# Kernel tuning notes

Hardware: AMD Instinct MI355X
Metric: run time of the kernel (lower is better)

The kernel has to match this reference:

```python
import jax, jax.numpy as jnp
import numpy as np

B, T, DIM, HEADS, DH = 4, 2048, 1024, 16, 64  # dh = dim // heads


def setup_inputs() -> dict:
    key = jax.random.key(0)
    k1, k2, k3 = jax.random.split(key, 3)
    x = jax.random.normal(k1, (B, T, DIM), dtype=jnp.float32)
    # nn.Linear weights, stored as [in, out] for x @ W convention
    W_qkv = jax.random.normal(k2, (DIM, 3 * HEADS * DH), dtype=jnp.float32) * (DIM ** -0.5)
    W_o = jax.random.normal(k3, (HEADS * DH, DIM), dtype=jnp.float32) * ((HEADS * DH) ** -0.5)
    return {"x": x, "W_qkv": W_qkv, "W_o": W_o}


def reference(x, W_qkv, W_o):
    b, t, _ = x.shape
    qkv = x @ W_qkv  # [b, t, 3*h*dh]
    # einops 'b t (d k h) -> k b h t d' with k=3, h=HEADS: fused axis splits as (dh, 3, h)
    qkv = qkv.reshape(b, t, DH, 3, HEADS)
    qkv = jnp.transpose(qkv, (3, 0, 4, 1, 2))  # [3, b, h, t, dh]
    q, k, v = qkv[0], qkv[1], qkv[2]
    scale = DH ** -0.5
    scores = jnp.einsum('bhid,bhjd->bhij', q, k) * scale  # [b, h, t, t]
    attn = jax.nn.softmax(scores, axis=-1)
    out = jnp.einsum('bhij,bhjd->bhid', attn, v)  # [b, h, t, dh]
    out = jnp.transpose(out, (0, 2, 1, 3)).reshape(b, t, HEADS * DH)  # 'b h t d -> b t (h d)'
    return out @ W_o
```

## Files before the change

### kernel.cpp

```cpp
#include <hip/hip_runtime.h>

typedef __bf16 bf16;
typedef __bf16 bf16x4 __attribute__((ext_vector_type(4)));
typedef __bf16 bf16x8 __attribute__((ext_vector_type(8)));
typedef float  f32x4  __attribute__((ext_vector_type(4)));
typedef unsigned int u32;
typedef unsigned int u32x2 __attribute__((ext_vector_type(2)));
typedef unsigned int u32x4 __attribute__((ext_vector_type(4)));

#define LOG2E 1.44269504088896340736f
#define EXP_SC (0.125f * LOG2E)

#if __has_builtin(__builtin_amdgcn_exp2f)
#define EXP2F(x) __builtin_amdgcn_exp2f(x)
#else
#define EXP2F(x) __builtin_exp2f(x)
#endif

__device__ __forceinline__ u32 pk_bf16(float lo, float hi) {
  u32 a = __float_as_uint(lo) + 0x8000u;
  u32 b = __float_as_uint(hi) + 0x8000u;
  return __builtin_amdgcn_perm(b, a, 0x07060302);
}
__device__ __forceinline__ unsigned short bf16r(float x) {
  return (unsigned short)((__float_as_uint(x) + 0x8000u) >> 16);
}

__device__ __forceinline__ void async_ld16(void* lds, const void* g) {
  __builtin_amdgcn_global_load_lds(
      (const __attribute__((address_space(1))) void*)(g),
      (__attribute__((address_space(3))) void*)(lds),
      16, 0, 0);
}

__global__ void convert_x(const float* __restrict__ x, bf16* __restrict__ xb) {
  int i = blockIdx.x * 256 + threadIdx.x;
  float4 v = ((const float4*)x)[i];
  u32x2 o = { pk_bf16(v.x, v.y), pk_bf16(v.z, v.w) };
  *(u32x2*)(xb + (size_t)i * 4) = o;
}

__global__ void prep_wqkv(const float* __restrict__ W, bf16* __restrict__ WT) {
  __shared__ float s[4 * 3072];
  const int k0 = blockIdx.x * 4;
  for (int i = threadIdx.x; i < 3072; i += 256) {
    int r = i / 768, c = (i - r * 768) * 4;
    *(float4*)(s + r * 3072 + c) = *(const float4*)(W + (size_t)(k0 + r) * 3072 + c);
  }
  __syncthreads();
  for (int n = threadIdx.x; n < 3072; n += 256) {
    int d = n & 63, h = (n >> 6) & 15, wch = n >> 10;
    int on = d * 48 + wch * 16 + h;
    u32x2 v = { pk_bf16(s[0 * 3072 + on], s[1 * 3072 + on]),
                pk_bf16(s[2 * 3072 + on], s[3 * 3072 + on]) };
    *(u32x2*)(WT + (size_t)n * 1024 + k0) = v;
  }
}

__global__ void prep_wo(const float* __restrict__ W, bf16* __restrict__ WT) {
  __shared__ float s[8 * 1024];
  const int k0 = blockIdx.x * 8;
  for (int i = threadIdx.x; i < 2048; i += 256) {
    int r = i >> 8, c = (i & 255) * 4;
    *(float4*)(s + r * 1024 + c) = *(const float4*)(W + (size_t)(k0 + r) * 1024 + c);
  }
  __syncthreads();
  for (int n = threadIdx.x; n < 1024; n += 256) {
    u32x4 v = { pk_bf16(s[0 * 1024 + n], s[1 * 1024 + n]),
                pk_bf16(s[2 * 1024 + n], s[3 * 1024 + n]),
                pk_bf16(s[4 * 1024 + n], s[5 * 1024 + n]),
                pk_bf16(s[6 * 1024 + n], s[7 * 1024 + n]) };
    *(u32x4*)(WT + (size_t)n * 1024 + k0) = v;
  }
}

template <int MODE>
__launch_bounds__(256, 2)
__global__ void gemm_bt(const bf16* __restrict__ A, const bf16* __restrict__ BT,
                        float* __restrict__ C, int N,
                        bf16* __restrict__ Qb, bf16* __restrict__ Kb, bf16* __restrict__ Vb) {
  constexpr int K = 1024;
  __shared__ bf16 sA[128 * 32];
  __shared__ bf16 sB[128 * 32];
  const int m0 = blockIdx.y * 128;
  const int n0 = blockIdx.x * 128;
  const int tid = threadIdx.x;
  const int lane = tid & 63;
  const int w = tid >> 6;
  const int wm = (w >> 1) * 64, wn = (w & 1) * 64;
  const int l15 = lane & 15, quad = lane >> 4;

  f32x4 acc[4][4];
  for (int i = 0; i < 4; i++)
    for (int j = 0; j < 4; j++) acc[i][j] = f32x4{0.f, 0.f, 0.f, 0.f};

  const int c0 = w * 128 + lane;
  const int c1 = c0 + 64;
  const int r0 = c0 >> 2, jg0 = (c0 & 3) ^ (r0 & 3);
  const int r1 = c1 >> 2, jg1 = (c1 & 3) ^ (r1 & 3);

  const bf16* gA0 = A  + (size_t)(m0 + r0) * K + jg0 * 8;
  const bf16* gA1 = A  + (size_t)(m0 + r1) * K + jg1 * 8;
  const bf16* gB0 = BT + (size_t)(n0 + r0) * K + jg0 * 8;
  const bf16* gB1 = BT + (size_t)(n0 + r1) * K + jg1 * 8;

  for (int k0 = 0; k0 < K; k0 += 32) {
    __syncthreads();
    async_ld16((void*)(sA + (w * 2) * 512),     gA0);
    async_ld16((void*)(sA + (w * 2 + 1) * 512), gA1);
    async_ld16((void*)(sB + (w * 2) * 512),     gB0);
    async_ld16((void*)(sB + (w * 2 + 1) * 512), gB1);
    gA0 += 32; gA1 += 32; gB0 += 32; gB1 += 32;
    __syncthreads();

    bf16x8 af[4], bfr[4];
    for (int ms = 0; ms < 4; ms++) {
      int r = wm + ms * 16 + l15;
      af[ms] = *(const bf16x8*)(sA + r * 32 + ((quad ^ (r & 3)) * 8));
    }
    for (int ns = 0; ns < 4; ns++) {
      int r = wn + ns * 16 + l15;
      bfr[ns] = *(const bf16x8*)(sB + r * 32 + ((quad ^ (r & 3)) * 8));
    }
    for (int ms = 0; ms < 4; ms++)
      for (int ns = 0; ns < 4; ns++)
        acc[ms][ns] = __builtin_amdgcn_mfma_f32_16x16x32_bf16(af[ms], bfr[ns], acc[ms][ns], 0, 0, 0);
  }

  if (MODE == 0) {
    for (int ms = 0; ms < 4; ms++)
      for (int ns = 0; ns < 4; ns++)
        for (int r = 0; r < 4; r++) {
          int row = m0 + wm + ms * 16 + quad * 4 + r;
          int col = n0 + wn + ns * 16 + l15;
          C[(size_t)row * N + col] = acc[ms][ns][r];
        }
  } else {
    for (int ms = 0; ms < 4; ms++)
      for (int ns = 0; ns < 4; ns++)
        for (int r = 0; r < 4; r++) {
          int row = m0 + wm + ms * 16 + quad * 4 + r;
          int col = n0 + wn + ns * 16 + l15;
          int b = row >> 11, t = row & 2047;
          int d = col & 63, h = (col >> 6) & 15, wch = col >> 10;
          bf16* dst = (wch == 0) ? Qb : (wch == 1) ? Kb : Vb;
          float v = acc[ms][ns][r] * ((wch == 0) ? EXP_SC : 1.0f);
          ((unsigned short*)dst)[(((size_t)(b * 16 + h)) * 2048 + t) * 64 + d] = bf16r(v);
        }
  }
}

__global__ void transpose_v(const bf16* __restrict__ V, bf16* __restrict__ VT) {
  __shared__ bf16 s[64 * 66];
  const int bh = blockIdx.y;
  const int t0 = blockIdx.x * 64;
  for (int i = threadIdx.x; i < 512; i += 256) {
    int t = i >> 3, dc = (i & 7) * 8;
    bf16x8 v = *(const bf16x8*)(V + ((size_t)bh * 2048 + t0 + t) * 64 + dc);
    for (int j = 0; j < 8; j++) s[t * 66 + dc + j] = v[j];
  }
  __syncthreads();
  for (int i = threadIdx.x; i < 512; i += 256) {
    int d = i >> 3, tc = (i & 7) * 8;
    bf16x8 v;
    for (int j = 0; j < 8; j++) {
      int kp = tc + j;
      int src = ((kp & 3) * 16) + (kp >> 2);
      v[j] = s[src * 66 + d];
    }
    *(bf16x8*)(VT + ((size_t)bh * 64 + d) * 2048 + t0 + tc) = v;
  }
}

__launch_bounds__(256, 2)
__global__ void attn_fwd(const bf16* __restrict__ Q, const bf16* __restrict__ K,
                         const bf16* __restrict__ VT, bf16* __restrict__ O) {
  __shared__ bf16 sK[64 * 64];
  __shared__ bf16 sV[64 * 64];
  __shared__ bf16 sP[4][32 * 64];
  const int bh = blockIdx.y;
  const int q0 = blockIdx.x * 128;
  const int tid = threadIdx.x;
  const int lane = tid & 63, w = tid >> 6;
  const int l15 = lane & 15, quad = lane >> 4;

  bf16x8 qf[2][2];
  for (int ms = 0; ms < 2; ms++)
    for (int kk = 0; kk < 2; kk++)
      qf[ms][kk] = *(const bf16x8*)(Q + ((size_t)bh * 2048 + q0 + w * 32 + ms * 16 + l15) * 64 + kk * 32 + quad * 8);

  f32x4 oa[2][4], lacc[2];
  for (int ms = 0; ms < 2; ms++) {
    for (int ds = 0; ds < 4; ds++) oa[ms][ds] = f32x4{0.f, 0.f, 0.f, 0.f};
    lacc[ms] = f32x4{0.f, 0.f, 0.f, 0.f};
  }
  bf16x8 onesf;
  for (int i = 0; i < 8; i++) onesf[i] = (bf16)1.0f;

  const int cA = w * 128 + lane;
  const int cB = cA + 64;
  const int rA = cA >> 3, jA = (cA & 7) ^ (rA & 7);
  const int rB = cB >> 3, jB = (cB & 7) ^ (rB & 7);
  const bf16* gKA = K  + ((size_t)bh * 2048 + rA) * 64 + jA * 8;
  const bf16* gKB = K  + ((size_t)bh * 2048 + rB) * 64 + jB * 8;
  const bf16* gVA = VT + ((size_t)bh * 64 + rA) * 2048 + jA * 8;
  const bf16* gVB = VT + ((size_t)bh * 64 + rB) * 2048 + jB * 8;

  int kvo[4][2], pfo[2][2], pwo[2][4];
  for (int ns = 0; ns < 4; ns++)
    for (int kk = 0; kk < 2; kk++) {
      int r = ns * 16 + l15;
      kvo[ns][kk] = r * 64 + (((kk * 4 + quad) ^ (r & 7)) * 8);
    }
  for (int ms = 0; ms < 2; ms++) {
    int r = ms * 16 + l15;
    for (int kk = 0; kk < 2; kk++)
      pfo[ms][kk] = r * 64 + (((kk * 4 + quad) ^ (r & 7)) * 8);
    for (int rr = 0; rr < 4; rr++) {
      int row = ms * 16 + quad * 4 + rr;
      pwo[ms][rr] = row * 64 + (((l15 >> 1) ^ (row & 7)) * 8) + (l15 & 1) * 4;
    }
  }

  for (int kt = 0; kt < 2048; kt += 64) {
    __syncthreads();
    async_ld16((void*)(sK + w * 1024),       gKA);
    async_ld16((void*)(sV + w * 1024),       gVA);
    async_ld16((void*)(sK + w * 1024 + 512), gKB);
    async_ld16((void*)(sV + w * 1024 + 512), gVB);
    gKA += 4096; gKB += 4096; gVA += 64; gVB += 64;
    __syncthreads();

    bf16x8 kf[4][2];
    for (int ns = 0; ns < 4; ns++)
      for (int kk = 0; kk < 2; kk++)
        kf[ns][kk] = *(const bf16x8*)(sK + kvo[ns][kk]);
    for (int ms = 0; ms < 2; ms++) {
      f32x4 s[4];
      for (int ns = 0; ns < 4; ns++) {
        f32x4 t = f32x4{0.f, 0.f, 0.f, 0.f};
        t = __builtin_amdgcn_mfma_f32_16x16x32_bf16(qf[ms][0], kf[ns][0], t, 0, 0, 0);
        t = __builtin_amdgcn_mfma_f32_16x16x32_bf16(qf[ms][1], kf[ns][1], t, 0, 0, 0);
        s[ns] = t;
      }
      for (int r = 0; r < 4; r++) {
        u32x2 pk = { pk_bf16(EXP2F(s[0][r]), EXP2F(s[1][r])),
                     pk_bf16(EXP2F(s[2][r]), EXP2F(s[3][r])) };
        *(u32x2*)(sP[w] + pwo[ms][r]) = pk;
      }
    }

    bf16x8 vf[4][2];
    for (int ds = 0; ds < 4; ds++)
      for (int kk = 0; kk < 2; kk++)
        vf[ds][kk] = *(const bf16x8*)(sV + kvo[ds][kk]);
    for (int ms = 0; ms < 2; ms++) {
      bf16x8 pf0 = *(const bf16x8*)(sP[w] + pfo[ms][0]);
      bf16x8 pf1 = *(const bf16x8*)(sP[w] + pfo[ms][1]);
      lacc[ms] = __builtin_amdgcn_mfma_f32_16x16x32_bf16(pf0, onesf, lacc[ms], 0, 0, 0);
      lacc[ms] = __builtin_amdgcn_mfma_f32_16x16x32_bf16(pf1, onesf, lacc[ms], 0, 0, 0);
      for (int ds = 0; ds < 4; ds++) {
        oa[ms][ds] = __builtin_amdgcn_mfma_f32_16x16x32_bf16(pf0, vf[ds][0], oa[ms][ds], 0, 0, 0);
        oa[ms][ds] = __builtin_amdgcn_mfma_f32_16x16x32_bf16(pf1, vf[ds][1], oa[ms][ds], 0, 0, 0);
      }
    }
  }

  const int b = bh >> 4, h = bh & 15;
  for (int ms = 0; ms < 2; ms++)
    for (int r = 0; r < 4; r++) {
      float inv = 1.0f / lacc[ms][r];
      int t = q0 + w * 32 + ms * 16 + quad * 4 + r;
      for (int ds = 0; ds < 4; ds++)
        ((unsigned short*)O)[((size_t)b * 2048 + t) * 1024 + h * 64 + ds * 16 + l15] =
            bf16r(oa[ms][ds][r] * inv);
    }
}

extern "C" void kernel_launch(void* const* d_in, const int* in_sizes, int n_in,
                              void* d_out, int out_size, void* d_ws, size_t ws_size,
                              hipStream_t stream) {
  const float* x    = (const float*)d_in[0];
  const float* Wqkv = (const float*)d_in[1];
  const float* Wo   = (const float*)d_in[2];
  float* out = (float*)d_out;
  char* ws = (char*)d_ws;

  bf16* wqkvT = (bf16*)(ws);
  bf16* woT   = (bf16*)(ws + 6291456);
  bf16* xb    = (bf16*)(ws + 8388608);
  bf16* Qb    = (bf16*)(ws + 25165824);
  bf16* Kb    = (bf16*)(ws + 41943040);
  bf16* Vb    = (bf16*)(ws + 58720256);
  bf16* VTb   = xb;
  bf16* AOb   = Vb;

  convert_x<<<8192, 256, 0, stream>>>(x, xb);
  prep_wqkv<<<256, 256, 0, stream>>>(Wqkv, wqkvT);
  prep_wo<<<128, 256, 0, stream>>>(Wo, woT);
  gemm_bt<1><<<dim3(24, 64), 256, 0, stream>>>(xb, wqkvT, nullptr, 3072, Qb, Kb, Vb);
  transpose_v<<<dim3(32, 64), 256, 0, stream>>>(Vb, VTb);
  attn_fwd<<<dim3(16, 64), 256, 0, stream>>>(Qb, Kb, VTb, AOb);
  gemm_bt<0><<<dim3(8, 64), 256, 0, stream>>>(AOb, woT, out, 1024, nullptr, nullptr, nullptr);
}
```

Baseline: 287.1 us.

## Double-buffer K/V tiles in LDS to overlap loads with attention compute

Makes the K and V shared-memory tiles double-buffered. The first tile is prefetched before the loop, and each iteration issues the async load for the next tile while the MFMA work runs on the current one. One of the two barriers per iteration goes away, so global-load latency no longer stalls the whole block between tiles. The cost is 16 KB more LDS per block, which could limit occupancy.

```diff
diff --git a/kernel.cpp b/kernel.cpp
--- a/kernel.cpp
+++ b/kernel.cpp
@@ -175,8 +175,8 @@
 __launch_bounds__(256, 2)
 __global__ void attn_fwd(const bf16* __restrict__ Q, const bf16* __restrict__ K,
                          const bf16* __restrict__ VT, bf16* __restrict__ O) {
-  __shared__ bf16 sK[64 * 64];
-  __shared__ bf16 sV[64 * 64];
+  __shared__ bf16 sK[2][64 * 64];
+  __shared__ bf16 sV[2][64 * 64];
   __shared__ bf16 sP[4][32 * 64];
   const int bh = blockIdx.y;
   const int q0 = blockIdx.x * 128;
@@ -222,19 +222,30 @@
     }
   }
 
-  for (int kt = 0; kt < 2048; kt += 64) {
+  async_ld16((void*)(sK[0] + w * 1024),       gKA);
+  async_ld16((void*)(sV[0] + w * 1024),       gVA);
+  async_ld16((void*)(sK[0] + w * 1024 + 512), gKB);
+  async_ld16((void*)(sV[0] + w * 1024 + 512), gVB);
+  gKA += 4096; gKB += 4096; gVA += 64; gVB += 64;
+
+  int buf = 0;
+  for (int it = 0; it < 32; it++) {
     __syncthreads();
-    async_ld16((void*)(sK + w * 1024),       gKA);
-    async_ld16((void*)(sV + w * 1024),       gVA);
-    async_ld16((void*)(sK + w * 1024 + 512), gKB);
-    async_ld16((void*)(sV + w * 1024 + 512), gVB);
-    gKA += 4096; gKB += 4096; gVA += 64; gVB += 64;
-    __syncthreads();
+    if (it < 31) {
+      int nb = buf ^ 1;
+      async_ld16((void*)(sK[nb] + w * 1024),       gKA);
+      async_ld16((void*)(sV[nb] + w * 1024),       gVA);
+      async_ld16((void*)(sK[nb] + w * 1024 + 512), gKB);
+      async_ld16((void*)(sV[nb] + w * 1024 + 512), gVB);
+      gKA += 4096; gKB += 4096; gVA += 64; gVB += 64;
+    }
+    const bf16* sKc = sK[buf];
+    const bf16* sVc = sV[buf];
 
     bf16x8 kf[4][2];
     for (int ns = 0; ns < 4; ns++)
       for (int kk = 0; kk < 2; kk++)
-        kf[ns][kk] = *(const bf16x8*)(sK + kvo[ns][kk]);
+        kf[ns][kk] = *(const bf16x8*)(sKc + kvo[ns][kk]);
     for (int ms = 0; ms < 2; ms++) {
       f32x4 s[4];
       for (int ns = 0; ns < 4; ns++) {
@@ -253,7 +264,7 @@
     bf16x8 vf[4][2];
     for (int ds = 0; ds < 4; ds++)
       for (int kk = 0; kk < 2; kk++)
-        vf[ds][kk] = *(const bf16x8*)(sV + kvo[ds][kk]);
+        vf[ds][kk] = *(const bf16x8*)(sVc + kvo[ds][kk]);
     for (int ms = 0; ms < 2; ms++) {
       bf16x8 pf0 = *(const bf16x8*)(sP[w] + pfo[ms][0]);
       bf16x8 pf1 = *(const bf16x8*)(sP[w] + pfo[ms][1]);
@@ -264,6 +275,7 @@
         oa[ms][ds] = __builtin_amdgcn_mfma_f32_16x16x32_bf16(pf1, vf[ds][1], oa[ms][ds], 0, 0, 0);
       }
     }
+    buf ^= 1;
   }
 
   const int b = bh >> 4, h = bh & 15;
```

Measured after the change: 297.3 us. 1.04x slower.

## Widen attention blocks to 8 waves and load 128-key tiles per barrier pair

Applied to the files above, without the earlier changes.

The attention kernel now runs 512 threads (8 waves) per block covering 256 queries and stages 128 keys of K and V^T per iteration, processed as two 64-key halves. This halves the number of __syncthreads pairs per key and shares each staged K/V tile across twice as many query rows. The manual round-and-pack into bf16 is also replaced with the hardware packed bf16 convert when that builtin exists. The cost is more LDS per block and fewer blocks in the grid (512), which may limit occupancy and latency hiding.

```diff
diff --git a/kernel.cpp b/kernel.cpp
--- a/kernel.cpp
+++ b/kernel.cpp
@@ -1,6 +1,7 @@
 #include <hip/hip_runtime.h>
 
 typedef __bf16 bf16;
+typedef __bf16 bf16x2 __attribute__((ext_vector_type(2)));
 typedef __bf16 bf16x4 __attribute__((ext_vector_type(4)));
 typedef __bf16 bf16x8 __attribute__((ext_vector_type(8)));
 typedef float  f32x4  __attribute__((ext_vector_type(4)));
@@ -22,6 +23,14 @@
   u32 b = __float_as_uint(hi) + 0x8000u;
   return __builtin_amdgcn_perm(b, a, 0x07060302);
 }
+#if __has_builtin(__builtin_amdgcn_cvt_pk_bf16_f32)
+__device__ __forceinline__ u32 cvtpk(float lo, float hi) {
+  bf16x2 t = __builtin_amdgcn_cvt_pk_bf16_f32(lo, hi);
+  return __builtin_bit_cast(u32, t);
+}
+#else
+__device__ __forceinline__ u32 cvtpk(float lo, float hi) { return pk_bf16(lo, hi); }
+#endif
 __device__ __forceinline__ unsigned short bf16r(float x) {
   return (unsigned short)((__float_as_uint(x) + 0x8000u) >> 16);
 }
@@ -172,14 +181,14 @@
   }
 }
 
-__launch_bounds__(256, 2)
+__launch_bounds__(512, 4)
 __global__ void attn_fwd(const bf16* __restrict__ Q, const bf16* __restrict__ K,
                          const bf16* __restrict__ VT, bf16* __restrict__ O) {
-  __shared__ bf16 sK[64 * 64];
-  __shared__ bf16 sV[64 * 64];
-  __shared__ bf16 sP[4][32 * 64];
+  __shared__ bf16 sK[2 * 64 * 64];
+  __shared__ bf16 sV[2 * 64 * 64];
+  __shared__ bf16 sP[8][32 * 64];
   const int bh = blockIdx.y;
-  const int q0 = blockIdx.x * 128;
+  const int q0 = blockIdx.x * 256;
   const int tid = threadIdx.x;
   const int lane = tid & 63, w = tid >> 6;
   const int l15 = lane & 15, quad = lane >> 4;
@@ -197,14 +206,10 @@
   bf16x8 onesf;
   for (int i = 0; i < 8; i++) onesf[i] = (bf16)1.0f;
 
-  const int cA = w * 128 + lane;
-  const int cB = cA + 64;
-  const int rA = cA >> 3, jA = (cA & 7) ^ (rA & 7);
-  const int rB = cB >> 3, jB = (cB & 7) ^ (rB & 7);
-  const bf16* gKA = K  + ((size_t)bh * 2048 + rA) * 64 + jA * 8;
-  const bf16* gKB = K  + ((size_t)bh * 2048 + rB) * 64 + jB * 8;
-  const bf16* gVA = VT + ((size_t)bh * 64 + rA) * 2048 + jA * 8;
-  const bf16* gVB = VT + ((size_t)bh * 64 + rB) * 2048 + jB * 8;
+  const int rS = tid >> 3;
+  const int jS = (tid & 7) ^ (rS & 7);
+  const bf16* gK = K  + ((size_t)bh * 2048 + rS) * 64 + jS * 8;
+  const bf16* gV = VT + ((size_t)bh * 64 + rS) * 2048 + jS * 8;
 
   int kvo[4][2], pfo[2][2], pwo[2][4];
   for (int ns = 0; ns < 4; ns++)
@@ -222,46 +227,51 @@
     }
   }
 
-  for (int kt = 0; kt < 2048; kt += 64) {
+  for (int kt = 0; kt < 2048; kt += 128) {
     __syncthreads();
-    async_ld16((void*)(sK + w * 1024),       gKA);
-    async_ld16((void*)(sV + w * 1024),       gVA);
-    async_ld16((void*)(sK + w * 1024 + 512), gKB);
-    async_ld16((void*)(sV + w * 1024 + 512), gVB);
-    gKA += 4096; gKB += 4096; gVA += 64; gVB += 64;
+    async_ld16((void*)(sK + (w * 64) * 8),         gK);
+    async_ld16((void*)(sK + (512 + w * 64) * 8),   gK + 4096);
+    async_ld16((void*)(sV + (w * 64) * 8),         gV);
+    async_ld16((void*)(sV + (512 + w * 64) * 8),   gV + 64);
+    gK += 8192; gV += 128;
     __syncthreads();
 
-    bf16x8 kf[4][2];
-    for (int ns = 0; ns < 4; ns++)
-      for (int kk = 0; kk < 2; kk++)
-        kf[ns][kk] = *(const bf16x8*)(sK + kvo[ns][kk]);
-    for (int ms = 0; ms < 2; ms++) {
-      f32x4 s[4];
-      for (int ns = 0; ns < 4; ns++) {
-        f32x4 t = f32x4{0.f, 0.f, 0.f, 0.f};
-        t = __builtin_amdgcn_mfma_f32_16x16x32_bf16(qf[ms][0], kf[ns][0], t, 0, 0, 0);
-        t = __builtin_amdgcn_mfma_f32_16x16x32_bf16(qf[ms][1], kf[ns][1], t, 0, 0, 0);
-        s[ns] = t;
+    for (int ht = 0; ht < 2; ht++) {
+      const bf16* sKc = sK + ht * 4096;
+      const bf16* sVc = sV + ht * 4096;
+
+      bf16x8 kf[4][2];
+      for (int ns = 0; ns < 4; ns++)
+        for (int kk = 0; kk < 2; kk++)
+          kf[ns][kk] = *(const bf16x8*)(sKc + kvo[ns][kk]);
+      for (int ms = 0; ms < 2; ms++) {
+        f32x4 s[4];
+        for (int ns = 0; ns < 4; ns++) {
+          f32x4 t = f32x4{0.f, 0.f, 0.f, 0.f};
+          t = __builtin_amdgcn_mfma_f32_16x16x32_bf16(qf[ms][0], kf[ns][0], t, 0, 0, 0);
+          t = __builtin_amdgcn_mfma_f32_16x16x32_bf16(qf[ms][1], kf[ns][1], t, 0, 0, 0);
+          s[ns] = t;
+        }
+        for (int r = 0; r < 4; r++) {
+          u32x2 pk = { cvtpk(EXP2F(s[0][r]), EXP2F(s[1][r])),
+                       cvtpk(EXP2F(s[2][r]), EXP2F(s[3][r])) };
+          *(u32x2*)(sP[w] + pwo[ms][r]) = pk;
+        }
       }
-      for (int r = 0; r < 4; r++) {
-        u32x2 pk = { pk_bf16(EXP2F(s[0][r]), EXP2F(s[1][r])),
-                     pk_bf16(EXP2F(s[2][r]), EXP2F(s[3][r])) };
-        *(u32x2*)(sP[w] + pwo[ms][r]) = pk;
-      }
-    }
-
-    bf16x8 vf[4][2];
-    for (int ds = 0; ds < 4; ds++)
-      for (int kk = 0; kk < 2; kk++)
-        vf[ds][kk] = *(const bf16x8*)(sV + kvo[ds][kk]);
-    for (int ms = 0; ms < 2; ms++) {
-      bf16x8 pf0 = *(const bf16x8*)(sP[w] + pfo[ms][0]);
-      bf16x8 pf1 = *(const bf16x8*)(sP[w] + pfo[ms][1]);
-      lacc[ms] = __builtin_amdgcn_mfma_f32_16x16x32_bf16(pf0, onesf, lacc[ms], 0, 0, 0);
-      lacc[ms] = __builtin_amdgcn_mfma_f32_16x16x32_bf16(pf1, onesf, lacc[ms], 0, 0, 0);
-      for (int ds = 0; ds < 4; ds++) {
-        oa[ms][ds] = __builtin_amdgcn_mfma_f32_16x16x32_bf16(pf0, vf[ds][0], oa[ms][ds], 0, 0, 0);
-        oa[ms][ds] = __builtin_amdgcn_mfma_f32_16x16x32_bf16(pf1, vf[ds][1], oa[ms][ds], 0, 0, 0);
+
+      bf16x8 vf[4][2];
+      for (int ds = 0; ds < 4; ds++)
+        for (int kk = 0; kk < 2; kk++)
+          vf[ds][kk] = *(const bf16x8*)(sVc + kvo[ds][kk]);
+      for (int ms = 0; ms < 2; ms++) {
+        bf16x8 pf0 = *(const bf16x8*)(sP[w] + pfo[ms][0]);
+        bf16x8 pf1 = *(const bf16x8*)(sP[w] + pfo[ms][1]);
+        lacc[ms] = __builtin_amdgcn_mfma_f32_16x16x32_bf16(pf0, onesf, lacc[ms], 0, 0, 0);
+        lacc[ms] = __builtin_amdgcn_mfma_f32_16x16x32_bf16(pf1, onesf, lacc[ms], 0, 0, 0);
+        for (int ds = 0; ds < 4; ds++) {
+          oa[ms][ds] = __builtin_amdgcn_mfma_f32_16x16x32_bf16(pf0, vf[ds][0], oa[ms][ds], 0, 0, 0);
+          oa[ms][ds] = __builtin_amdgcn_mfma_f32_16x16x32_bf16(pf1, vf[ds][1], oa[ms][ds], 0, 0, 0);
+        }
       }
     }
   }
@@ -300,6 +310,6 @@
   prep_wo<<<128, 256, 0, stream>>>(Wo, woT);
   gemm_bt<1><<<dim3(24, 64), 256, 0, stream>>>(xb, wqkvT, nullptr, 3072, Qb, Kb, Vb);
   transpose_v<<<dim3(32, 64), 256, 0, stream>>>(Vb, VTb);
-  attn_fwd<<<dim3(16, 64), 256, 0, stream>>>(Qb, Kb, VTb, AOb);
+  attn_fwd<<<dim3(8, 64), 512, 0, stream>>>(Qb, Kb, VTb, AOb);
   gemm_bt<0><<<dim3(8, 64), 256, 0, stream>>>(AOb, woT, out, 1024, nullptr, nullptr, nullptr);
 }
```

Result: no change. 292.1 us (+1.7%).
